# Kernel tuning notes

Measured on AMD Instinct MI355X. Metric: run time of the kernel, lower is better.

The kernel has to match this reference:

```python
import jax, jax.numpy as jnp
import numpy as np

B, N, NODE_DIM, COND_DIM, EDGE_DIM = 16, 256, 512, 512, 128
E_TOT = 262144  # total edges, divisible by B
EPS = 1e-5


def weight_norm(v, g):
    # torch weight_norm dim=0: per-output-row normalization. v: [out, in], g: [out]
    return v * (g / jnp.sqrt(jnp.sum(v * v, axis=1)))[:, None]


def setup_inputs() -> dict:
    key = jax.random.key(0)
    ks = jax.random.split(key, 12)
    node_feats = jax.random.normal(ks[0], (B, N, NODE_DIM), dtype=jnp.float32)
    cond_feats = jax.random.normal(ks[1], (B, COND_DIM), dtype=jnp.float32)
    edge_indexes = jnp.sort(jax.random.randint(ks[2], (E_TOT,), 0, B * N * N, dtype=jnp.int64))
    s_node = 1.0 / np.sqrt(NODE_DIM)
    s_cond = 1.0 / np.sqrt(COND_DIM)
    s_film = 1.0 / np.sqrt(2 * EDGE_DIM)
    return {
        "node_feats": node_feats,
        "cond_feats": cond_feats,
        "edge_indexes": edge_indexes,
        "v_node": jax.random.uniform(ks[3], (EDGE_DIM, NODE_DIM), jnp.float32, -s_node, s_node),
        "g_node": jnp.ones((EDGE_DIM,), jnp.float32),
        "b_node": jnp.zeros((EDGE_DIM,), jnp.float32),
        "v_cond": jax.random.uniform(ks[4], (2 * EDGE_DIM, COND_DIM), jnp.float32, -s_cond, s_cond),
        "g_cond": jnp.ones((2 * EDGE_DIM,), jnp.float32),
        "b_cond": jnp.zeros((2 * EDGE_DIM,), jnp.float32),
        "w_film": jax.random.uniform(ks[5], (EDGE_DIM, 2 * EDGE_DIM), jnp.float32, -s_film, s_film),
        "b_film": jnp.zeros((EDGE_DIM,), jnp.float32),
    }


def reference(node_feats, cond_feats, edge_indexes, v_node, g_node, b_node,
              v_cond, g_cond, b_cond, w_film, b_film):
    # node projection: Dropout(0) -> weight_norm Linear -> ReLU
    w_n = weight_norm(v_node, g_node)
    nodes = jax.nn.relu(jnp.einsum('bnd,ed->bne', node_feats, w_n) + b_node)  # [B,N,E]

    # cond projection -> gamma, beta
    w_c = weight_norm(v_cond, g_cond)
    gb = cond_feats @ w_c.T + b_cond  # [B, 2E]
    gamma = gb[:, :EDGE_DIM] + 1.0
    beta = gb[:, EDGE_DIM:]

    # gather edge endpoints directly (equivalent to materializing [B,N,N,2E] 'cat' then indexing)
    b_idx = edge_indexes // (N * N)
    i_idx = (edge_indexes // N) % N
    j_idx = edge_indexes % N
    fused = jnp.concatenate([nodes[b_idx, i_idx], nodes[b_idx, j_idx]], axis=-1)  # [E_TOT, 2E]

    # film_l: linear -> LayerNorm(no affine) -> FiLM -> ReLU, on view (B, E_TOT//B, E)
    x = fused @ w_film.T + b_film  # [E_TOT, EDGE_DIM]
    x = x.reshape(B, E_TOT // B, EDGE_DIM)
    mu = jnp.mean(x, axis=-1, keepdims=True)
    var = jnp.mean(jnp.square(x - mu), axis=-1, keepdims=True)
    x = (x - mu) * jax.lax.rsqrt(var + EPS)
    x = x * gamma[:, None, :] + beta[:, None, :]
    x = jax.nn.relu(x)
    return x.reshape(E_TOT, EDGE_DIM)
```

## Files before the change

### kernel.cpp

```cpp
#include <hip/hip_runtime.h>
#include <hip/hip_bf16.h>

typedef __bf16 bf16_t;
typedef bf16_t bf16x8 __attribute__((ext_vector_type(8)));
typedef bf16_t bf16x4 __attribute__((ext_vector_type(4)));
typedef float f32x4 __attribute__((ext_vector_type(4)));

#define NODE_DIM 512
#define COND_DIM 512
#define EDGE_DIM 128

#define WS_A    0x000000
#define WS_WN   0x400000
#define WS_WC   0x420000
#define WS_SC   0x430000
#define WS_GA   0x431000
#define WS_BE   0x433000
#define WS_P    0x440000

__device__ __forceinline__ bf16x8 cvt8(float4 a, float4 b) {
    bf16x8 v;
    v[0] = (bf16_t)a.x; v[1] = (bf16_t)a.y; v[2] = (bf16_t)a.z; v[3] = (bf16_t)a.w;
    v[4] = (bf16_t)b.x; v[5] = (bf16_t)b.y; v[6] = (bf16_t)b.z; v[7] = (bf16_t)b.w;
    return v;
}

__global__ __launch_bounds__(256) void prep_kernel(
    const float* __restrict__ node_feats, const float* __restrict__ cond_feats,
    const float* __restrict__ v_node, const float* __restrict__ g_node,
    const float* __restrict__ v_cond, const float* __restrict__ g_cond,
    const float* __restrict__ b_cond, const float* __restrict__ w_film,
    char* __restrict__ ws)
{
    bf16_t* A  = (bf16_t*)(ws + WS_A);
    bf16_t* Wn = (bf16_t*)(ws + WS_WN);
    bf16_t* Wc = (bf16_t*)(ws + WS_WC);
    float* scale_node = (float*)(ws + WS_SC);
    float* gamma = (float*)(ws + WS_GA);
    float* beta  = (float*)(ws + WS_BE);

    int t = threadIdx.x;
    int bid = blockIdx.x;
    int lane = t & 63, wv = t >> 6;

    if (bid < 1024) {
        size_t idx = ((size_t)bid * 256 + t) * 8;
        float4 a = ((const float4*)(node_feats + idx))[0];
        float4 b = ((const float4*)(node_feats + idx))[1];
        *(bf16x8*)(A + idx) = cvt8(a, b);
    } else if (bid < 1056) {
        size_t idx = ((size_t)(bid - 1024) * 256 + t) * 8;
        float4 a = ((const float4*)(v_node + idx))[0];
        float4 b = ((const float4*)(v_node + idx))[1];
        *(bf16x8*)(Wn + idx) = cvt8(a, b);
    } else if (bid < 1072) {
        int u = (bid - 1056) * 256 + t;
        int n = u >> 4;
        int ko = (u & 15) * 8;
        const float* src = (n < 128) ? (w_film + (size_t)n * 256 + ko)
                                     : (w_film + (size_t)(n - 128) * 256 + 128 + ko);
        float4 a = ((const float4*)src)[0];
        float4 b = ((const float4*)src)[1];
        *(bf16x8*)(Wc + (size_t)n * 128 + ko) = cvt8(a, b);
    } else if (bid < 1104) {
        int id = (bid - 1072) * 4 + wv;
        const float* vn = v_node + (size_t)id * NODE_DIM + lane * 8;
        float sq = 0.f;
#pragma unroll
        for (int i = 0; i < 2; i++) {
            float4 v4 = ((const float4*)vn)[i];
            sq += v4.x * v4.x + v4.y * v4.y + v4.z * v4.z + v4.w * v4.w;
        }
#pragma unroll
        for (int o = 32; o > 0; o >>= 1) sq += __shfl_xor(sq, o);
        if (lane == 0) scale_node[id] = g_node[id] * rsqrtf(sq);
    } else {
        int id = (bid - 1104) * 4 + wv;
        int b = id >> 8, n = id & 255;
        const float* cf = cond_feats + b * COND_DIM + lane * 8;
        const float* vc = v_cond + (size_t)n * COND_DIM + lane * 8;
        float dot = 0.f, sq = 0.f;
#pragma unroll
        for (int i = 0; i < 2; i++) {
            float4 c4 = ((const float4*)cf)[i];
            float4 v4 = ((const float4*)vc)[i];
            dot += c4.x * v4.x + c4.y * v4.y + c4.z * v4.z + c4.w * v4.w;
            sq  += v4.x * v4.x + v4.y * v4.y + v4.z * v4.z + v4.w * v4.w;
        }
#pragma unroll
        for (int o = 32; o > 0; o >>= 1) {
            dot += __shfl_xor(dot, o);
            sq  += __shfl_xor(sq, o);
        }
        if (lane == 0) {
            float val = dot * (g_cond[n] * rsqrtf(sq)) + b_cond[n];
            if (n < 128) gamma[b * 128 + n] = val + 1.0f;
            else         beta[b * 128 + (n - 128)] = val;
        }
    }
}

__global__ __launch_bounds__(256) void gemm_kernel(
    const float* __restrict__ b_node, char* __restrict__ ws)
{
    const bf16_t* A  = (const bf16_t*)(ws + WS_A);
    const bf16_t* Wn = (const bf16_t*)(ws + WS_WN);
    const bf16_t* Wc = (const bf16_t*)(ws + WS_WC);
    const float* scale_node = (const float*)(ws + WS_SC);
    bf16_t* P = (bf16_t*)(ws + WS_P);

    __shared__ __attribute__((aligned(16))) bf16_t N_s[16 * 136];
    __shared__ __attribute__((aligned(16))) float  T_s[4][16][68];

    int t = threadIdx.x;
    int lane = t & 63, w = t >> 6;
    int r16 = lane & 15, half = lane >> 4;
    int m0 = blockIdx.x * 16;

    f32x4 zero4 = {0.f, 0.f, 0.f, 0.f};

    f32x4 acc0 = zero4, acc1 = zero4;
    {
        const bf16_t* aptr = A + (size_t)(m0 + r16) * NODE_DIM + half * 8;
        const bf16_t* bptr = Wn + (size_t)(w * 32 + r16) * NODE_DIM + half * 8;
#pragma unroll
        for (int ks = 0; ks < 16; ks++) {
            bf16x8 af = *(const bf16x8*)(aptr + ks * 32);
            bf16x8 b0 = *(const bf16x8*)(bptr + ks * 32);
            bf16x8 b1 = *(const bf16x8*)(bptr + 16 * NODE_DIM + ks * 32);
            acc0 = __builtin_amdgcn_mfma_f32_16x16x32_bf16(af, b0, acc0, 0, 0, 0);
            acc1 = __builtin_amdgcn_mfma_f32_16x16x32_bf16(af, b1, acc1, 0, 0, 0);
        }
    }
    {
        int rbase = half * 4;
#pragma unroll
        for (int j = 0; j < 2; j++) {
            int col = w * 32 + j * 16 + r16;
            float s = scale_node[col], bb = b_node[col];
            f32x4 a = j ? acc1 : acc0;
#pragma unroll
            for (int r = 0; r < 4; r++) {
                float v = fmaxf(a[r] * s + bb, 0.f);
                N_s[(rbase + r) * 136 + col] = (bf16_t)v;
            }
        }
    }
    __syncthreads();

    f32x4 acc2[4];
#pragma unroll
    for (int i = 0; i < 4; i++) acc2[i] = zero4;
    {
        const bf16_t* bptr = Wc + (size_t)(w * 64 + r16) * 128 + half * 8;
#pragma unroll
        for (int ks = 0; ks < 4; ks++) {
            bf16x8 af = *(const bf16x8*)&N_s[r16 * 136 + ks * 32 + half * 8];
#pragma unroll
            for (int j = 0; j < 4; j++) {
                bf16x8 bf = *(const bf16x8*)(bptr + j * 16 * 128 + ks * 32);
                acc2[j] = __builtin_amdgcn_mfma_f32_16x16x32_bf16(af, bf, acc2[j], 0, 0, 0);
            }
        }
    }
    {
        int rbase = half * 4;
#pragma unroll
        for (int j = 0; j < 4; j++) {
            int col = j * 16 + r16;
#pragma unroll
            for (int r = 0; r < 4; r++) T_s[w][rbase + r][col] = acc2[j][r];
        }
    }
    __syncthreads();
    {
#pragma unroll
        for (int r2 = 0; r2 < 2; r2++) {
            int row = r2 * 8 + (lane >> 3);
            int colg = (lane & 7) * 8;
            float4 a = *(const float4*)&T_s[w][row][colg];
            float4 b = *(const float4*)&T_s[w][row][colg + 4];
            *(bf16x8*)&P[(size_t)(m0 + row) * 256 + w * 64 + colg] = cvt8(a, b);
        }
    }
}

__global__ __launch_bounds__(256) void edge_kernel(
    const int* __restrict__ edges, const char* __restrict__ ws,
    const float* __restrict__ b_film, float* __restrict__ out)
{
    const bf16_t* P = (const bf16_t*)(ws + WS_P);
    const float* gamma = (const float*)(ws + WS_GA);
    const float* beta  = (const float*)(ws + WS_BE);

    int t = threadIdx.x;
    int lane = t & 63, wv = t >> 6;
    int v = (blockIdx.x & 7) * 4096 + (blockIdx.x >> 3);
    int r = v * 8 + wv * 2 + (lane >> 5);
    int hl = lane & 31;
    int c = hl * 4;

    int bb = v >> 11;
    float4 g4  = *(const float4*)&gamma[bb * 128 + c];
    float4 be4 = *(const float4*)&beta[bb * 128 + c];
    float4 bf4 = *(const float4*)&b_film[c];

    int e = edges[r];
    int ri = e >> 8;
    int rj = ((e >> 16) << 8) | (e & 255);

    bf16x4 p1 = *(const bf16x4*)&P[(size_t)ri * 256 + c];
    bf16x4 p2 = *(const bf16x4*)&P[(size_t)rj * 256 + 128 + c];

    float x0 = (float)p1[0] + (float)p2[0] + bf4.x;
    float x1 = (float)p1[1] + (float)p2[1] + bf4.y;
    float x2 = (float)p1[2] + (float)p2[2] + bf4.z;
    float x3 = (float)p1[3] + (float)p2[3] + bf4.w;

    float s  = x0 + x1 + x2 + x3;
    float ss = x0 * x0 + x1 * x1 + x2 * x2 + x3 * x3;
#pragma unroll
    for (int o = 16; o > 0; o >>= 1) {
        s  += __shfl_xor(s, o);
        ss += __shfl_xor(ss, o);
    }
    float mu  = s * (1.0f / 128.0f);
    float var = ss * (1.0f / 128.0f) - mu * mu;
    float rs  = rsqrtf(var + 1e-5f);

    float4 o4;
    o4.x = fmaxf((x0 - mu) * rs * g4.x + be4.x, 0.f);
    o4.y = fmaxf((x1 - mu) * rs * g4.y + be4.y, 0.f);
    o4.z = fmaxf((x2 - mu) * rs * g4.z + be4.z, 0.f);
    o4.w = fmaxf((x3 - mu) * rs * g4.w + be4.w, 0.f);
    *(float4*)&out[(size_t)r * 128 + c] = o4;
}

extern "C" void kernel_launch(void* const* d_in, const int* in_sizes, int n_in,
                              void* d_out, int out_size, void* d_ws, size_t ws_size,
                              hipStream_t stream) {
    const float* node_feats = (const float*)d_in[0];
    const float* cond_feats = (const float*)d_in[1];
    const int*   edges      = (const int*)d_in[2];
    const float* v_node     = (const float*)d_in[3];
    const float* g_node     = (const float*)d_in[4];
    const float* b_node     = (const float*)d_in[5];
    const float* v_cond     = (const float*)d_in[6];
    const float* g_cond     = (const float*)d_in[7];
    const float* b_cond     = (const float*)d_in[8];
    const float* w_film     = (const float*)d_in[9];
    const float* b_film     = (const float*)d_in[10];
    float* out = (float*)d_out;
    char* ws = (char*)d_ws;

    prep_kernel<<<2128, 256, 0, stream>>>(node_feats, cond_feats, v_node, g_node,
                                          v_cond, g_cond, b_cond, w_film, ws);
    gemm_kernel<<<256, 256, 0, stream>>>(b_node, ws);
    edge_kernel<<<32768, 256, 0, stream>>>(edges, ws, b_film, out);
}
```

Baseline: 197.2 us.

## Fuse node_feats bf16 conversion into GEMM and widen edge kernel per-thread work

```diff
diff --git a/kernel.cpp b/kernel.cpp
--- a/kernel.cpp
+++ b/kernel.cpp
@@ -10,13 +10,12 @@
 #define COND_DIM 512
 #define EDGE_DIM 128
 
-#define WS_A    0x000000
-#define WS_WN   0x400000
-#define WS_WC   0x420000
-#define WS_SC   0x430000
-#define WS_GA   0x431000
-#define WS_BE   0x433000
-#define WS_P    0x440000
+#define WS_WN   0x000000
+#define WS_WC   0x020000
+#define WS_SC   0x030000
+#define WS_GA   0x031000
+#define WS_BE   0x033000
+#define WS_P    0x040000
 
 __device__ __forceinline__ bf16x8 cvt8(float4 a, float4 b) {
     bf16x8 v;
@@ -26,13 +25,12 @@
 }
 
 __global__ __launch_bounds__(256) void prep_kernel(
-    const float* __restrict__ node_feats, const float* __restrict__ cond_feats,
+    const float* __restrict__ cond_feats,
     const float* __restrict__ v_node, const float* __restrict__ g_node,
     const float* __restrict__ v_cond, const float* __restrict__ g_cond,
     const float* __restrict__ b_cond, const float* __restrict__ w_film,
     char* __restrict__ ws)
 {
-    bf16_t* A  = (bf16_t*)(ws + WS_A);
     bf16_t* Wn = (bf16_t*)(ws + WS_WN);
     bf16_t* Wc = (bf16_t*)(ws + WS_WC);
     float* scale_node = (float*)(ws + WS_SC);
@@ -43,18 +41,13 @@
     int bid = blockIdx.x;
     int lane = t & 63, wv = t >> 6;
 
-    if (bid < 1024) {
+    if (bid < 32) {
         size_t idx = ((size_t)bid * 256 + t) * 8;
-        float4 a = ((const float4*)(node_feats + idx))[0];
-        float4 b = ((const float4*)(node_feats + idx))[1];
-        *(bf16x8*)(A + idx) = cvt8(a, b);
-    } else if (bid < 1056) {
-        size_t idx = ((size_t)(bid - 1024) * 256 + t) * 8;
         float4 a = ((const float4*)(v_node + idx))[0];
         float4 b = ((const float4*)(v_node + idx))[1];
         *(bf16x8*)(Wn + idx) = cvt8(a, b);
-    } else if (bid < 1072) {
-        int u = (bid - 1056) * 256 + t;
+    } else if (bid < 48) {
+        int u = (bid - 32) * 256 + t;
         int n = u >> 4;
         int ko = (u & 15) * 8;
         const float* src = (n < 128) ? (w_film + (size_t)n * 256 + ko)
@@ -62,8 +55,8 @@
         float4 a = ((const float4*)src)[0];
         float4 b = ((const float4*)src)[1];
         *(bf16x8*)(Wc + (size_t)n * 128 + ko) = cvt8(a, b);
-    } else if (bid < 1104) {
-        int id = (bid - 1072) * 4 + wv;
+    } else if (bid < 80) {
+        int id = (bid - 48) * 4 + wv;
         const float* vn = v_node + (size_t)id * NODE_DIM + lane * 8;
         float sq = 0.f;
 #pragma unroll
@@ -75,7 +68,7 @@
         for (int o = 32; o > 0; o >>= 1) sq += __shfl_xor(sq, o);
         if (lane == 0) scale_node[id] = g_node[id] * rsqrtf(sq);
     } else {
-        int id = (bid - 1104) * 4 + wv;
+        int id = (bid - 80) * 4 + wv;
         int b = id >> 8, n = id & 255;
         const float* cf = cond_feats + b * COND_DIM + lane * 8;
         const float* vc = v_cond + (size_t)n * COND_DIM + lane * 8;
@@ -101,9 +94,9 @@
 }
 
 __global__ __launch_bounds__(256) void gemm_kernel(
-    const float* __restrict__ b_node, char* __restrict__ ws)
+    const float* __restrict__ node_feats, const float* __restrict__ b_node,
+    char* __restrict__ ws)
 {
-    const bf16_t* A  = (const bf16_t*)(ws + WS_A);
     const bf16_t* Wn = (const bf16_t*)(ws + WS_WN);
     const bf16_t* Wc = (const bf16_t*)(ws + WS_WC);
     const float* scale_node = (const float*)(ws + WS_SC);
@@ -121,11 +114,13 @@
 
     f32x4 acc0 = zero4, acc1 = zero4;
     {
-        const bf16_t* aptr = A + (size_t)(m0 + r16) * NODE_DIM + half * 8;
+        const float*  aptr = node_feats + (size_t)(m0 + r16) * NODE_DIM + half * 8;
         const bf16_t* bptr = Wn + (size_t)(w * 32 + r16) * NODE_DIM + half * 8;
 #pragma unroll
         for (int ks = 0; ks < 16; ks++) {
-            bf16x8 af = *(const bf16x8*)(aptr + ks * 32);
+            float4 a0 = ((const float4*)(aptr + ks * 32))[0];
+            float4 a1 = ((const float4*)(aptr + ks * 32))[1];
+            bf16x8 af = cvt8(a0, a1);
             bf16x8 b0 = *(const bf16x8*)(bptr + ks * 32);
             bf16x8 b1 = *(const bf16x8*)(bptr + 16 * NODE_DIM + ks * 32);
             acc0 = __builtin_amdgcn_mfma_f32_16x16x32_bf16(af, b0, acc0, 0, 0, 0);
@@ -194,46 +189,64 @@
     const float* beta  = (const float*)(ws + WS_BE);
 
     int t = threadIdx.x;
-    int lane = t & 63, wv = t >> 6;
-    int v = (blockIdx.x & 7) * 4096 + (blockIdx.x >> 3);
-    int r = v * 8 + wv * 2 + (lane >> 5);
-    int hl = lane & 31;
-    int c = hl * 4;
-
-    int bb = v >> 11;
-    float4 g4  = *(const float4*)&gamma[bb * 128 + c];
-    float4 be4 = *(const float4*)&beta[bb * 128 + c];
-    float4 bf4 = *(const float4*)&b_film[c];
-
-    int e = edges[r];
-    int ri = e >> 8;
-    int rj = ((e >> 16) << 8) | (e & 255);
-
-    bf16x4 p1 = *(const bf16x4*)&P[(size_t)ri * 256 + c];
-    bf16x4 p2 = *(const bf16x4*)&P[(size_t)rj * 256 + 128 + c];
-
-    float x0 = (float)p1[0] + (float)p2[0] + bf4.x;
-    float x1 = (float)p1[1] + (float)p2[1] + bf4.y;
-    float x2 = (float)p1[2] + (float)p2[2] + bf4.z;
-    float x3 = (float)p1[3] + (float)p2[3] + bf4.w;
-
-    float s  = x0 + x1 + x2 + x3;
-    float ss = x0 * x0 + x1 * x1 + x2 * x2 + x3 * x3;
-#pragma unroll
-    for (int o = 16; o > 0; o >>= 1) {
-        s  += __shfl_xor(s, o);
-        ss += __shfl_xor(ss, o);
-    }
-    float mu  = s * (1.0f / 128.0f);
-    float var = ss * (1.0f / 128.0f) - mu * mu;
-    float rs  = rsqrtf(var + 1e-5f);
-
-    float4 o4;
-    o4.x = fmaxf((x0 - mu) * rs * g4.x + be4.x, 0.f);
-    o4.y = fmaxf((x1 - mu) * rs * g4.y + be4.y, 0.f);
-    o4.z = fmaxf((x2 - mu) * rs * g4.z + be4.z, 0.f);
-    o4.w = fmaxf((x3 - mu) * rs * g4.w + be4.w, 0.f);
-    *(float4*)&out[(size_t)r * 128 + c] = o4;
+    int l16  = t & 15;
+    int rsub = t >> 4;
+    int c = l16 * 8;
+
+    int base = (blockIdx.x & 7) * 32768 + (blockIdx.x >> 3) * 32;
+    int bb = base >> 14;
+
+    float4 g0  = *(const float4*)&gamma[bb * 128 + c];
+    float4 g1  = *(const float4*)&gamma[bb * 128 + c + 4];
+    float4 be0 = *(const float4*)&beta[bb * 128 + c];
+    float4 be1 = *(const float4*)&beta[bb * 128 + c + 4];
+    float4 bf0 = *(const float4*)&b_film[c];
+    float4 bf1 = *(const float4*)&b_film[c + 4];
+
+#pragma unroll
+    for (int it = 0; it < 2; it++) {
+        int r = base + it * 16 + rsub;
+        int e = edges[r];
+        int ri = e >> 8;
+        int rj = ((e >> 16) << 8) | (e & 255);
+
+        bf16x8 p1 = *(const bf16x8*)&P[(size_t)ri * 256 + c];
+        bf16x8 p2 = *(const bf16x8*)&P[(size_t)rj * 256 + 128 + c];
+
+        float x0 = (float)p1[0] + (float)p2[0] + bf0.x;
+        float x1 = (float)p1[1] + (float)p2[1] + bf0.y;
+        float x2 = (float)p1[2] + (float)p2[2] + bf0.z;
+        float x3 = (float)p1[3] + (float)p2[3] + bf0.w;
+        float x4 = (float)p1[4] + (float)p2[4] + bf1.x;
+        float x5 = (float)p1[5] + (float)p2[5] + bf1.y;
+        float x6 = (float)p1[6] + (float)p2[6] + bf1.z;
+        float x7 = (float)p1[7] + (float)p2[7] + bf1.w;
+
+        float s  = ((x0 + x1) + (x2 + x3)) + ((x4 + x5) + (x6 + x7));
+        float ss = x0 * x0 + x1 * x1 + x2 * x2 + x3 * x3
+                 + x4 * x4 + x5 * x5 + x6 * x6 + x7 * x7;
+#pragma unroll
+        for (int m = 8; m >= 1; m >>= 1) {
+            s  += __shfl_xor(s, m);
+            ss += __shfl_xor(ss, m);
+        }
+        float mu  = s * (1.0f / 128.0f);
+        float var = ss * (1.0f / 128.0f) - mu * mu;
+        float rs  = rsqrtf(var + 1e-5f);
+
+        f32x4 o0, o1;
+        o0[0] = fmaxf((x0 - mu) * rs * g0.x + be0.x, 0.f);
+        o0[1] = fmaxf((x1 - mu) * rs * g0.y + be0.y, 0.f);
+        o0[2] = fmaxf((x2 - mu) * rs * g0.z + be0.z, 0.f);
+        o0[3] = fmaxf((x3 - mu) * rs * g0.w + be0.w, 0.f);
+        o1[0] = fmaxf((x4 - mu) * rs * g1.x + be1.x, 0.f);
+        o1[1] = fmaxf((x5 - mu) * rs * g1.y + be1.y, 0.f);
+        o1[2] = fmaxf((x6 - mu) * rs * g1.z + be1.z, 0.f);
+        o1[3] = fmaxf((x7 - mu) * rs * g1.w + be1.w, 0.f);
+
+        __builtin_nontemporal_store(o0, (f32x4*)&out[(size_t)r * 128 + c]);
+        __builtin_nontemporal_store(o1, (f32x4*)&out[(size_t)r * 128 + c + 4]);
+    }
 }
 
 extern "C" void kernel_launch(void* const* d_in, const int* in_sizes, int n_in,
@@ -253,8 +266,8 @@
     float* out = (float*)d_out;
     char* ws = (char*)d_ws;
 
-    prep_kernel<<<2128, 256, 0, stream>>>(node_feats, cond_feats, v_node, g_node,
+    prep_kernel<<<1104, 256, 0, stream>>>(cond_feats, v_node, g_node,
                                           v_cond, g_cond, b_cond, w_film, ws);
-    gemm_kernel<<<256, 256, 0, stream>>>(b_node, ws);
-    edge_kernel<<<32768, 256, 0, stream>>>(edges, ws, b_film, out);
-}
+    gemm_kernel<<<256, 256, 0, stream>>>(node_feats, b_node, ws);
+    edge_kernel<<<8192, 256, 0, stream>>>(edges, ws, b_film, out);
+}
```

Result: faster. 190.9 us (-3.2%).
